# Kernel tuning notes

Measured on AMD Instinct MI355X. Metric: run time of the kernel, lower is better.

## Reference

```python
import jax, jax.numpy as jnp
import numpy as np

CHUNK = 128  # chunk size for the causal linear-attention recurrence
EPS = 1e-10


def _causal_numerator(q, k, v, chunk=CHUNK):
    """N_i = sum_{j<=i} (q_i . k_j) v_j, computed chunk-recurrently.

    q,k: [B,H,N,D]; v: [B,H,N,E] -> [B,H,N,E]
    """
    B, H, N, D = q.shape
    E = v.shape[-1]
    nc = N // chunk
    qc = jnp.moveaxis(q.reshape(B, H, nc, chunk, D), 2, 0)  # [nc,B,H,c,D]
    kc = jnp.moveaxis(k.reshape(B, H, nc, chunk, D), 2, 0)
    vc = jnp.moveaxis(v.reshape(B, H, nc, chunk, E), 2, 0)
    mask = jnp.tril(jnp.ones((chunk, chunk), dtype=q.dtype))  # causal within chunk

    def step(S, inp):  # S: running sum of k_j (outer) v_j -> [B,H,D,E]
        qi, ki, vi = inp
        scores = jnp.einsum('bhid,bhjd->bhij', qi, ki) * mask
        intra = jnp.einsum('bhij,bhje->bhie', scores, vi)
        inter = jnp.einsum('bhid,bhde->bhie', qi, S)
        S = S + jnp.einsum('bhjd,bhje->bhde', ki, vi)
        return S, intra + inter

    S0 = jnp.zeros((B, H, D, E), q.dtype)
    _, outs = jax.lax.scan(step, S0, (qc, kc, vc))  # [nc,B,H,c,E]
    return jnp.moveaxis(outs, 0, 2).reshape(B, H, N, E)


def _causal_denominator(q, k):
    # D_i = q_i . cumsum_j<=i k_j  -> [B,H,N]
    return jnp.einsum('bhnd,bhnd->bhn', q, jnp.cumsum(k, axis=-2))


def setup_inputs() -> dict:
    key = jax.random.key(0)
    ks = jax.random.split(key, 5)
    shape = (2, 8, 4096, 64)
    names = ['q', 'k', 'q_rot', 'k_rot', 'v']
    # feature-mapped inputs (Performer softmax features) are positive
    return {n: jax.random.uniform(ks[i], shape, dtype=jnp.float32) for i, n in enumerate(names)}


def reference(q, k, q_rot, k_rot, v):
    N = _causal_numerator(q, k, v) + _causal_numerator(q_rot, k_rot, v)
    D = _causal_denominator(q, k) + _causal_denominator(q_rot, k_rot)
    return N * (1.0 / (D + EPS))[..., None]
```

## Files before the change

kernel.cpp:

```cpp
#include <hip/hip_runtime.h>

#define SEQ 4096
#define DIM 64
#define CHUNK 128
#define NC 32
#define EPSV 1e-10f
#define KS_OFF 4194304

typedef __attribute__((ext_vector_type(8))) short s16x8;
typedef __attribute__((ext_vector_type(4))) float f32x4;

__device__ __forceinline__ unsigned short f2bf(float f) {
  unsigned int u = __float_as_uint(f);
  u += 0x7FFF + ((u >> 16) & 1);
  return (unsigned short)(u >> 16);
}
__device__ __forceinline__ float bf2f(unsigned short s) {
  return __uint_as_float(((unsigned int)s) << 16);
}

__global__ __launch_bounds__(256) void pass_a(const float* __restrict__ k0,
                                              const float* __restrict__ k1,
                                              const float* __restrict__ v,
                                              float* __restrict__ ws) {
  __shared__ __align__(16) unsigned short skT[64 * 136];
  __shared__ __align__(16) unsigned short svT[64 * 136];
  int bid = blockIdx.x;
  int m = bid >> 9, rem = bid & 511, hh = rem >> 5, c = rem & 31;
  const float* kp = (m ? k1 : k0) + (size_t)hh * SEQ * DIM + (size_t)c * CHUNK * DIM;
  const float* vp = v + (size_t)hh * SEQ * DIM + (size_t)c * CHUNK * DIM;
  int t = threadIdx.x;

  for (int pass = 0; pass < 8; ++pass) {
    int idx = t + pass * 256;
    int j = idx >> 4, e4 = idx & 15;
    float4 kk = ((const float4*)kp)[idx];
    float4 vv = ((const float4*)vp)[idx];
    int d0 = e4 * 4;
    skT[(d0 + 0) * 136 + j] = f2bf(kk.x);
    skT[(d0 + 1) * 136 + j] = f2bf(kk.y);
    skT[(d0 + 2) * 136 + j] = f2bf(kk.z);
    skT[(d0 + 3) * 136 + j] = f2bf(kk.w);
    svT[(d0 + 0) * 136 + j] = f2bf(vv.x);
    svT[(d0 + 1) * 136 + j] = f2bf(vv.y);
    svT[(d0 + 2) * 136 + j] = f2bf(vv.z);
    svT[(d0 + 3) * 136 + j] = f2bf(vv.w);
  }
  __syncthreads();

  if (t < 64) {
    float s = 0.f;
    for (int it = 0; it < 16; ++it) {
      s16x8 blk = *(const s16x8*)&skT[t * 136 + it * 8];
#pragma unroll
      for (int u = 0; u < 8; ++u) s += bf2f((unsigned short)blk[u]);
    }
    ws[KS_OFF + (size_t)bid * 64 + t] = s;
  }

  int w = t >> 6, L = t & 63, g = L >> 4, cL = L & 15;
  f32x4 acc[4];
#pragma unroll
  for (int ct = 0; ct < 4; ++ct) acc[ct] = (f32x4){0.f, 0.f, 0.f, 0.f};
#pragma unroll
  for (int ks = 0; ks < 4; ++ks) {
    s16x8 aF = *(const s16x8*)&svT[(w * 16 + cL) * 136 + ks * 32 + g * 8];
#pragma unroll
    for (int ct = 0; ct < 4; ++ct) {
      s16x8 bF = *(const s16x8*)&skT[(ct * 16 + cL) * 136 + ks * 32 + g * 8];
      acc[ct] = __builtin_amdgcn_mfma_f32_16x16x32_bf16(aF, bF, acc[ct], 0, 0, 0);
    }
  }
  float* Sp = ws + (size_t)bid * 4096;
#pragma unroll
  for (int ct = 0; ct < 4; ++ct)
#pragma unroll
    for (int r = 0; r < 4; ++r)
      Sp[(size_t)(w * 16 + g * 4 + r) * 64 + ct * 16 + cL] = acc[ct][r];
}

__global__ __launch_bounds__(256) void pass_b(float* __restrict__ ws) {
  int t = blockIdx.x * 256 + threadIdx.x;
  if (blockIdx.x < 512) {
    int mh = t >> 12, de = t & 4095;
    float* p = ws + (size_t)mh * NC * 4096 + de;
    float run = 0.f;
    for (int c = 0; c < NC; ++c) {
      float x = p[(size_t)c * 4096];
      p[(size_t)c * 4096] = run;
      run += x;
    }
  } else {
    int t2 = t - 512 * 256;
    int mh = t2 >> 6, d = t2 & 63;
    float* p = ws + KS_OFF + (size_t)mh * NC * 64 + d;
    float run = 0.f;
    for (int c = 0; c < NC; ++c) {
      float x = p[(size_t)c * 64];
      p[(size_t)c * 64] = run;
      run += x;
    }
  }
}

__global__ __launch_bounds__(256) void pass_c(const float* __restrict__ q0,
                                              const float* __restrict__ q1,
                                              const float* __restrict__ k0,
                                              const float* __restrict__ k1,
                                              const float* __restrict__ v,
                                              const float* __restrict__ ws,
                                              float* __restrict__ out) {
  __shared__ __align__(16) unsigned short sq[128 * 72];
  __shared__ __align__(16) unsigned short skl[128 * 72];
  __shared__ __align__(16) unsigned short svT[64 * 136];
  __shared__ __align__(16) unsigned short sU[5120];
  __shared__ float sden[128];
  __shared__ float skpref[64];

  int hh = blockIdx.x >> 5, c = blockIdx.x & 31;
  int t = threadIdx.x;
  int w = t >> 6, L = t & 63, g = L >> 4, cL = L & 15;
  size_t off = (size_t)hh * SEQ * DIM + (size_t)c * CHUNK * DIM;

  const float* vp = v + off;
  for (int pass = 0; pass < 8; ++pass) {
    int idx = t + pass * 256;
    int j = idx >> 4, e4 = idx & 15;
    float4 vv = ((const float4*)vp)[idx];
    int e0 = e4 * 4;
    svT[(e0 + 0) * 136 + j] = f2bf(vv.x);
    svT[(e0 + 1) * 136 + j] = f2bf(vv.y);
    svT[(e0 + 2) * 136 + j] = f2bf(vv.z);
    svT[(e0 + 3) * 136 + j] = f2bf(vv.w);
  }

  f32x4 accO[2][4];
#pragma unroll
  for (int a = 0; a < 2; ++a)
#pragma unroll
    for (int b = 0; b < 4; ++b) accO[a][b] = (f32x4){0.f, 0.f, 0.f, 0.f};
  float denfrag[2][4] = {};
  float denqk = 0.f;

  for (int m = 0; m < 2; ++m) {
    const float* qp = (m ? q1 : q0) + off;
    const float* kp = (m ? k1 : k0) + off;
    const float* Sp = ws + (size_t)(m * 512 + hh * 32 + c) * 4096;
    const float* Kp = ws + KS_OFF + (size_t)(m * 512 + hh * 32 + c) * 64;

    __syncthreads();
    for (int pass = 0; pass < 8; ++pass) {
      int idx = t + pass * 256;
      int i = idx >> 4, d4 = idx & 15;
      float4 qq = ((const float4*)qp)[idx];
      float4 kk = ((const float4*)kp)[idx];
      ushort4 uq = make_ushort4(f2bf(qq.x), f2bf(qq.y), f2bf(qq.z), f2bf(qq.w));
      ushort4 uk = make_ushort4(f2bf(kk.x), f2bf(kk.y), f2bf(kk.z), f2bf(kk.w));
      *(ushort4*)&sq[i * 72 + d4 * 4] = uq;
      *(ushort4*)&skl[i * 72 + d4 * 4] = uk;
    }
    for (int pass = 0; pass < 4; ++pass) {
      int idx = t + pass * 256;
      int e = idx >> 4, d4 = idx & 15;
      float4 ss = ((const float4*)Sp)[idx];
      ushort4 us = make_ushort4(f2bf(ss.x), f2bf(ss.y), f2bf(ss.z), f2bf(ss.w));
      *(ushort4*)&sU[e * 72 + d4 * 4] = us;
    }
    if (t < 64) skpref[t] = Kp[t];
    __syncthreads();

    s16x8 aq[2][2];
#pragma unroll
    for (int rt01 = 0; rt01 < 2; ++rt01) {
      int row = (2 * w + rt01) * 16 + cL;
      aq[rt01][0] = *(const s16x8*)&sq[row * 72 + g * 8];
      aq[rt01][1] = *(const s16x8*)&sq[row * 72 + 32 + g * 8];
    }

    if (t < 128) {
      float s = 0.f;
      for (int it = 0; it < 8; ++it) {
        s16x8 blk = *(const s16x8*)&sq[t * 72 + it * 8];
#pragma unroll
        for (int u = 0; u < 8; ++u) s += bf2f((unsigned short)blk[u]) * skpref[it * 8 + u];
      }
      denqk += s;
    }

#pragma unroll
    for (int h = 0; h < 2; ++h) {
#pragma unroll
      for (int et = 0; et < 4; ++et) {
        s16x8 bS = *(const s16x8*)&sU[(et * 16 + cL) * 72 + h * 32 + g * 8];
        accO[0][et] = __builtin_amdgcn_mfma_f32_16x16x32_bf16(aq[0][h], bS, accO[0][et], 0, 0, 0);
        accO[1][et] = __builtin_amdgcn_mfma_f32_16x16x32_bf16(aq[1][h], bS, accO[1][et], 0, 0, 0);
      }
    }
    __syncthreads();

    for (int s = 0; s <= w; ++s) {
      s16x8 bK[2][2];
#pragma unroll
      for (int ct01 = 0; ct01 < 2; ++ct01) {
        int jrow = (2 * s + ct01) * 16 + cL;
        bK[ct01][0] = *(const s16x8*)&skl[jrow * 72 + g * 8];
        bK[ct01][1] = *(const s16x8*)&skl[jrow * 72 + 32 + g * 8];
      }
#pragma unroll
      for (int rt01 = 0; rt01 < 2; ++rt01) {
        int rt = 2 * w + rt01;
        int rowbase = rt * 16 + g * 4;
#pragma unroll
        for (int ct01 = 0; ct01 < 2; ++ct01) {
          int jt = 2 * s + ct01;
          if (jt > rt) {
#pragma unroll
            for (int r = 0; r < 4; ++r) sU[(rowbase + r) * 40 + ct01 * 16 + cL] = 0;
          } else {
            f32x4 C = (f32x4){0.f, 0.f, 0.f, 0.f};
            C = __builtin_amdgcn_mfma_f32_16x16x32_bf16(aq[rt01][0], bK[ct01][0], C, 0, 0, 0);
            C = __builtin_amdgcn_mfma_f32_16x16x32_bf16(aq[rt01][1], bK[ct01][1], C, 0, 0, 0);
            if (jt == rt) {
#pragma unroll
              for (int r = 0; r < 4; ++r)
                if (cL > g * 4 + r) C[r] = 0.f;
            }
#pragma unroll
            for (int r = 0; r < 4; ++r) {
              denfrag[rt01][r] += C[r];
              sU[(rowbase + r) * 40 + ct01 * 16 + cL] = f2bf(C[r]);
            }
          }
        }
      }
      asm volatile("s_waitcnt lgkmcnt(0)" ::: "memory");

      s16x8 bV[4];
#pragma unroll
      for (int et = 0; et < 4; ++et)
        bV[et] = *(const s16x8*)&svT[(et * 16 + cL) * 136 + s * 32 + g * 8];
#pragma unroll
      for (int rt01 = 0; rt01 < 2; ++rt01) {
        s16x8 aP = *(const s16x8*)&sU[((2 * w + rt01) * 16 + cL) * 40 + g * 8];
#pragma unroll
        for (int et = 0; et < 4; ++et)
          accO[rt01][et] = __builtin_amdgcn_mfma_f32_16x16x32_bf16(aP, bV[et], accO[rt01][et], 0, 0, 0);
      }
    }
  }

  if (t < 128) sden[t] = denqk;
  __syncthreads();

  float* op = out + off;
#pragma unroll
  for (int rt01 = 0; rt01 < 2; ++rt01) {
#pragma unroll
    for (int r = 0; r < 4; ++r) {
      float vs = denfrag[rt01][r];
      vs += __shfl_xor(vs, 1);
      vs += __shfl_xor(vs, 2);
      vs += __shfl_xor(vs, 4);
      vs += __shfl_xor(vs, 8);
      int row = (2 * w + rt01) * 16 + g * 4 + r;
      float inv = 1.f / (sden[row] + vs + EPSV);
#pragma unroll
      for (int et = 0; et < 4; ++et)
        op[(size_t)row * 64 + et * 16 + cL] = accO[rt01][et][r] * inv;
    }
  }
}

extern "C" void kernel_launch(void* const* d_in, const int* in_sizes, int n_in,
                              void* d_out, int out_size, void* d_ws, size_t ws_size,
                              hipStream_t stream) {
  const float* q  = (const float*)d_in[0];
  const float* k  = (const float*)d_in[1];
  const float* qr = (const float*)d_in[2];
  const float* kr = (const float*)d_in[3];
  const float* v  = (const float*)d_in[4];
  float* out = (float*)d_out;
  float* ws  = (float*)d_ws;

  hipLaunchKernelGGL(pass_a, dim3(1024), dim3(256), 0, stream, k, kr, v, ws);
  hipLaunchKernelGGL(pass_b, dim3(520), dim3(256), 0, stream, ws);
  hipLaunchKernelGGL(pass_c, dim3(512), dim3(256), 0, stream, q, qr, k, kr, v, ws, out);
}
```

Baseline: 144.3 us.

## Balance causal tiles across waves and stage transposes through natural-layout LDS

Each wave in pass_c now owns row tiles w and 7-w instead of two adjacent tiles, so the triangular causal work is spread evenly across the four waves rather than the last wave doing most of it. The scattered per-element transposed LDS stores of K and V are replaced by coalesced ushort4 stores into a natural-layout buffer, followed by a separate LDS transpose pass that writes 16-byte segments. The transpose adds extra barriers and LDS traffic, and pass_a needs an additional shared buffer, which may lower occupancy.

```diff
diff --git a/kernel.cpp b/kernel.cpp
--- a/kernel.cpp
+++ b/kernel.cpp
@@ -19,33 +19,51 @@
   return __uint_as_float(((unsigned int)s) << 16);
 }
 
+__device__ __forceinline__ void stage_nat(const float* __restrict__ gp,
+                                          unsigned short* __restrict__ nat, int t) {
+#pragma unroll
+  for (int p = 0; p < 8; ++p) {
+    int idx = t + p * 256;
+    int i = idx >> 4, d4 = idx & 15;
+    float4 x = ((const float4*)gp)[idx];
+    ushort4 u = make_ushort4(f2bf(x.x), f2bf(x.y), f2bf(x.z), f2bf(x.w));
+    *(ushort4*)&nat[i * 72 + d4 * 4] = u;
+  }
+}
+
+__device__ __forceinline__ void transpose_to_T(const unsigned short* __restrict__ nat,
+                                               unsigned short* __restrict__ dst, int t) {
+  int L = t & 63, w = t >> 6;
+#pragma unroll
+  for (int it = 0; it < 4; ++it) {
+    int d = L, j8 = it * 4 + w;
+    s16x8 seg;
+#pragma unroll
+    for (int u = 0; u < 8; ++u) seg[u] = (short)nat[(j8 * 8 + u) * 72 + d];
+    *(s16x8*)&dst[d * 136 + j8 * 8] = seg;
+  }
+}
+
 __global__ __launch_bounds__(256) void pass_a(const float* __restrict__ k0,
                                               const float* __restrict__ k1,
                                               const float* __restrict__ v,
                                               float* __restrict__ ws) {
   __shared__ __align__(16) unsigned short skT[64 * 136];
   __shared__ __align__(16) unsigned short svT[64 * 136];
+  __shared__ __align__(16) unsigned short snat[128 * 72];
   int bid = blockIdx.x;
   int m = bid >> 9, rem = bid & 511, hh = rem >> 5, c = rem & 31;
   const float* kp = (m ? k1 : k0) + (size_t)hh * SEQ * DIM + (size_t)c * CHUNK * DIM;
   const float* vp = v + (size_t)hh * SEQ * DIM + (size_t)c * CHUNK * DIM;
   int t = threadIdx.x;
 
-  for (int pass = 0; pass < 8; ++pass) {
-    int idx = t + pass * 256;
-    int j = idx >> 4, e4 = idx & 15;
-    float4 kk = ((const float4*)kp)[idx];
-    float4 vv = ((const float4*)vp)[idx];
-    int d0 = e4 * 4;
-    skT[(d0 + 0) * 136 + j] = f2bf(kk.x);
-    skT[(d0 + 1) * 136 + j] = f2bf(kk.y);
-    skT[(d0 + 2) * 136 + j] = f2bf(kk.z);
-    skT[(d0 + 3) * 136 + j] = f2bf(kk.w);
-    svT[(d0 + 0) * 136 + j] = f2bf(vv.x);
-    svT[(d0 + 1) * 136 + j] = f2bf(vv.y);
-    svT[(d0 + 2) * 136 + j] = f2bf(vv.z);
-    svT[(d0 + 3) * 136 + j] = f2bf(vv.w);
-  }
+  stage_nat(kp, snat, t);
+  __syncthreads();
+  transpose_to_T(snat, skT, t);
+  __syncthreads();
+  stage_nat(vp, snat, t);
+  __syncthreads();
+  transpose_to_T(snat, svT, t);
   __syncthreads();
 
   if (t < 64) {
@@ -121,18 +139,11 @@
   int t = threadIdx.x;
   int w = t >> 6, L = t & 63, g = L >> 4, cL = L & 15;
   size_t off = (size_t)hh * SEQ * DIM + (size_t)c * CHUNK * DIM;
-
-  const float* vp = v + off;
-  for (int pass = 0; pass < 8; ++pass) {
-    int idx = t + pass * 256;
-    int j = idx >> 4, e4 = idx & 15;
-    float4 vv = ((const float4*)vp)[idx];
-    int e0 = e4 * 4;
-    svT[(e0 + 0) * 136 + j] = f2bf(vv.x);
-    svT[(e0 + 1) * 136 + j] = f2bf(vv.y);
-    svT[(e0 + 2) * 136 + j] = f2bf(vv.z);
-    svT[(e0 + 3) * 136 + j] = f2bf(vv.w);
-  }
+  int rt_of[2] = {w, 7 - w};
+
+  stage_nat(v + off, skl, t);
+  __syncthreads();
+  transpose_to_T(skl, svT, t);
 
   f32x4 accO[2][4];
 #pragma unroll
@@ -149,16 +160,9 @@
     const float* Kp = ws + KS_OFF + (size_t)(m * 512 + hh * 32 + c) * 64;
 
     __syncthreads();
-    for (int pass = 0; pass < 8; ++pass) {
-      int idx = t + pass * 256;
-      int i = idx >> 4, d4 = idx & 15;
-      float4 qq = ((const float4*)qp)[idx];
-      float4 kk = ((const float4*)kp)[idx];
-      ushort4 uq = make_ushort4(f2bf(qq.x), f2bf(qq.y), f2bf(qq.z), f2bf(qq.w));
-      ushort4 uk = make_ushort4(f2bf(kk.x), f2bf(kk.y), f2bf(kk.z), f2bf(kk.w));
-      *(ushort4*)&sq[i * 72 + d4 * 4] = uq;
-      *(ushort4*)&skl[i * 72 + d4 * 4] = uk;
-    }
+    stage_nat(qp, sq, t);
+    stage_nat(kp, skl, t);
+#pragma unroll
     for (int pass = 0; pass < 4; ++pass) {
       int idx = t + pass * 256;
       int e = idx >> 4, d4 = idx & 15;
@@ -171,10 +175,10 @@
 
     s16x8 aq[2][2];
 #pragma unroll
-    for (int rt01 = 0; rt01 < 2; ++rt01) {
-      int row = (2 * w + rt01) * 16 + cL;
-      aq[rt01][0] = *(const s16x8*)&sq[row * 72 + g * 8];
-      aq[rt01][1] = *(const s16x8*)&sq[row * 72 + 32 + g * 8];
+    for (int ti = 0; ti < 2; ++ti) {
+      int row = rt_of[ti] * 16 + cL;
+      aq[ti][0] = *(const s16x8*)&sq[row * 72 + g * 8];
+      aq[ti][1] = *(const s16x8*)&sq[row * 72 + 32 + g * 8];
     }
 
     if (t < 128) {
@@ -198,7 +202,7 @@
     }
     __syncthreads();
 
-    for (int s = 0; s <= w; ++s) {
+    for (int s = 0; s <= (7 - w) >> 1; ++s) {
       s16x8 bK[2][2];
 #pragma unroll
       for (int ct01 = 0; ct01 < 2; ++ct01) {
@@ -207,8 +211,9 @@
         bK[ct01][1] = *(const s16x8*)&skl[jrow * 72 + 32 + g * 8];
       }
 #pragma unroll
-      for (int rt01 = 0; rt01 < 2; ++rt01) {
-        int rt = 2 * w + rt01;
+      for (int ti = 0; ti < 2; ++ti) {
+        int rt = rt_of[ti];
+        if (2 * s > rt) continue;
         int rowbase = rt * 16 + g * 4;
 #pragma unroll
         for (int ct01 = 0; ct01 < 2; ++ct01) {
@@ -218,8 +223,8 @@
             for (int r = 0; r < 4; ++r) sU[(rowbase + r) * 40 + ct01 * 16 + cL] = 0;
           } else {
             f32x4 C = (f32x4){0.f, 0.f, 0.f, 0.f};
-            C = __builtin_amdgcn_mfma_f32_16x16x32_bf16(aq[rt01][0], bK[ct01][0], C, 0, 0, 0);
-            C = __builtin_amdgcn_mfma_f32_16x16x32_bf16(aq[rt01][1], bK[ct01][1], C, 0, 0, 0);
+            C = __builtin_amdgcn_mfma_f32_16x16x32_bf16(aq[ti][0], bK[ct01][0], C, 0, 0, 0);
+            C = __builtin_amdgcn_mfma_f32_16x16x32_bf16(aq[ti][1], bK[ct01][1], C, 0, 0, 0);
             if (jt == rt) {
 #pragma unroll
               for (int r = 0; r < 4; ++r)
@@ -227,7 +232,7 @@
             }
 #pragma unroll
             for (int r = 0; r < 4; ++r) {
-              denfrag[rt01][r] += C[r];
+              denfrag[ti][r] += C[r];
               sU[(rowbase + r) * 40 + ct01 * 16 + cL] = f2bf(C[r]);
             }
           }
@@ -240,11 +245,12 @@
       for (int et = 0; et < 4; ++et)
         bV[et] = *(const s16x8*)&svT[(et * 16 + cL) * 136 + s * 32 + g * 8];
 #pragma unroll
-      for (int rt01 = 0; rt01 < 2; ++rt01) {
-        s16x8 aP = *(const s16x8*)&sU[((2 * w + rt01) * 16 + cL) * 40 + g * 8];
+      for (int ti = 0; ti < 2; ++ti) {
+        if (2 * s > rt_of[ti]) continue;
+        s16x8 aP = *(const s16x8*)&sU[(rt_of[ti] * 16 + cL) * 40 + g * 8];
 #pragma unroll
         for (int et = 0; et < 4; ++et)
-          accO[rt01][et] = __builtin_amdgcn_mfma_f32_16x16x32_bf16(aP, bV[et], accO[rt01][et], 0, 0, 0);
+          accO[ti][et] = __builtin_amdgcn_mfma_f32_16x16x32_bf16(aP, bV[et], accO[ti][et], 0, 0, 0);
       }
     }
   }
@@ -254,19 +260,19 @@
 
   float* op = out + off;
 #pragma unroll
-  for (int rt01 = 0; rt01 < 2; ++rt01) {
+  for (int ti = 0; ti < 2; ++ti) {
 #pragma unroll
     for (int r = 0; r < 4; ++r) {
-      float vs = denfrag[rt01][r];
+      float vs = denfrag[ti][r];
       vs += __shfl_xor(vs, 1);
       vs += __shfl_xor(vs, 2);
       vs += __shfl_xor(vs, 4);
       vs += __shfl_xor(vs, 8);
-      int row = (2 * w + rt01) * 16 + g * 4 + r;
+      int row = rt_of[ti] * 16 + g * 4 + r;
       float inv = 1.f / (sden[row] + vs + EPSV);
 #pragma unroll
       for (int et = 0; et < 4; ++et)
-        op[(size_t)row * 64 + et * 16 + cL] = accO[rt01][et][r] * inv;
+        op[(size_t)row * 64 + et * 16 + cL] = accO[ti][et][r] * inv;
     }
   }
 }
```

Measured after the change: 143.7 us. Within noise of the previous version (-0.4%).
